# Optimization experiments

Hardware: AMD Instinct MI355X
Metric: run time of the kernel (lower is better)

Reference implementation:

```python
import jax, jax.numpy as jnp
import numpy as np

AH, AW = 7, 7            # alignedHeight, alignedWidth
SCALE = 0.0625           # spatialScale = 1/16


def setup_inputs() -> dict:
    key = jax.random.key(0)
    k1, k2, k3, k4 = jax.random.split(key, 4)
    B, C, H, W, K = 4, 1024, 50, 50, 512
    features = jax.random.normal(k1, (B, C, H, W), dtype=jnp.float32)
    bidx = jax.random.randint(k2, (K, 1), 0, B).astype(jnp.float32)
    xs = jnp.sort(jax.random.uniform(k3, (K, 2), minval=0.0, maxval=799.0), axis=1)
    ys = jnp.sort(jax.random.uniform(k4, (K, 2), minval=0.0, maxval=799.0), axis=1)
    # rois: (batch_idx, x1, y1, x2, y2) in image coords
    rois = jnp.concatenate([bidx, xs[:, 0:1], ys[:, 0:1], xs[:, 1:2], ys[:, 1:2]], axis=1)
    return {"features": features, "rois": rois}


def _roi_align(features, rois):
    # legacy roi_align: grid of (AH+1)x(AW+1) points, bin = extent/(grid-1),
    # one bilinear sample per grid point, zero outside feature map.
    B, C, H, W = features.shape
    bidx = rois[:, 0].astype(jnp.int32)
    x1 = rois[:, 1] * SCALE
    y1 = rois[:, 2] * SCALE
    x2 = rois[:, 3] * SCALE
    y2 = rois[:, 4] * SCALE
    bh = jnp.maximum(y2 - y1, 0.0) / AH  # (AH+1)-1 grid intervals
    bw = jnp.maximum(x2 - x1, 0.0) / AW
    ys = y1[:, None] + jnp.arange(AH + 1, dtype=jnp.float32) * bh[:, None]  # [K,AH+1]
    xs = x1[:, None] + jnp.arange(AW + 1, dtype=jnp.float32) * bw[:, None]  # [K,AW+1]
    yg = ys[:, :, None]   # [K,AH+1,1]
    xg = xs[:, None, :]   # [K,1,AW+1]
    valid = (yg >= 0) & (yg < H) & (xg >= 0) & (xg < W)   # [K,AH+1,AW+1]
    y0 = jnp.clip(jnp.floor(yg), 0, H - 2).astype(jnp.int32)
    x0 = jnp.clip(jnp.floor(xg), 0, W - 2).astype(jnp.int32)
    wy = yg - y0.astype(jnp.float32)  # [K,AH+1,1]
    wx = xg - x0.astype(jnp.float32)  # [K,1,AW+1]
    b = bidx[:, None, None]
    # gathered corners: [K, AH+1, AW+1, C]
    v00 = features[b, :, y0, x0]
    v01 = features[b, :, y0, x0 + 1]
    v10 = features[b, :, y0 + 1, x0]
    v11 = features[b, :, y0 + 1, x0 + 1]
    out = (v00 * ((1 - wy) * (1 - wx))[..., None]
           + v01 * ((1 - wy) * wx)[..., None]
           + v10 * (wy * (1 - wx))[..., None]
           + v11 * (wy * wx)[..., None])
    out = jnp.where(valid[..., None], out, 0.0)
    return jnp.transpose(out, (0, 3, 1, 2))  # [K, C, AH+1, AW+1]


def reference(features, rois):
    a = _roi_align(features, rois)
    # avg_pool2d(kernel=2, stride=1) -> [K, C, AH, AW]
    pooled = (a[..., :-1, :-1] + a[..., 1:, :-1] + a[..., :-1, 1:] + a[..., 1:, 1:]) * 0.25
    return pooled
```

## Files before the change

kernel.cpp:

```cpp
#include <hip/hip_runtime.h>

#define K_ROIS   512
#define BATCH    4
#define CHANNELS 1024
#define FH       50
#define FW       50
#define AH       7
#define AW       7
#define SCALE_F  0.0625f
#define CPT      4


__global__ void roi_prep(const float* __restrict__ rois,
                         int* __restrict__ cnt,
                         int* __restrict__ roiIdx,
                         float4* __restrict__ paramsS) {
    int r = blockIdx.x * blockDim.x + threadIdx.x;
    if (r >= K_ROIS) return;
    float bf = rois[r * 5 + 0];
    float x1 = rois[r * 5 + 1] * SCALE_F;
    float y1 = rois[r * 5 + 2] * SCALE_F;
    float x2 = rois[r * 5 + 3] * SCALE_F;
    float y2 = rois[r * 5 + 4] * SCALE_F;
    float bw = fmaxf(x2 - x1, 0.f) * (1.f / (float)AW);
    float bh = fmaxf(y2 - y1, 0.f) * (1.f / (float)AH);
    int ib = (int)bf;
    int pos = atomicAdd(&cnt[ib], 1);
    roiIdx[ib * K_ROIS + pos] = r;
    paramsS[ib * K_ROIS + pos] = make_float4(x1, y1, bw, bh);
}

__global__ __launch_bounds__(256)
void roi_pool(const float* __restrict__ feat,
              const int* __restrict__ cnt,
              const int* __restrict__ roiIdx,
              const float4* __restrict__ paramsS,
              float* __restrict__ out) {
    __shared__ float4 patch4[FH * FW];

    const int b  = blockIdx.x & 3;
    const int c0 = (blockIdx.x >> 2) * CPT;

    const float* pl = feat + ((size_t)b * CHANNELS + c0) * (FH * FW);
    for (int idx = threadIdx.x; idx < FH * FW; idx += 256) {
        float4 v;
        v.x = pl[idx];
        v.y = pl[idx + FH * FW];
        v.z = pl[idx + 2 * FH * FW];
        v.w = pl[idx + 3 * FH * FW];
        patch4[idx] = v;
    }
    __syncthreads();

    const int lane = threadIdx.x & 63;
    const int wv   = threadIdx.x >> 6;
    const int j = lane >> 3;
    const int i = lane & 7;
    const float jf = (float)j;
    const float iff = (float)i;
    const bool do_out = (j < AH) && (i < AW);
    const int outoff = j * AW + i;

    const int n = cnt[b];
    const int base = b * K_ROIS;

    int rr = wv;
    float4 pp = make_float4(0.f, 0.f, 0.f, 0.f);
    int roi = 0;
    if (rr < n) { pp = paramsS[base + rr]; roi = roiIdx[base + rr]; }

    while (rr < n) {
        const int rn = rr + 4;
        float4 ppn = pp;
        int roin = roi;
        if (rn < n) { ppn = paramsS[base + rn]; roin = roiIdx[base + rn]; }

        const float xg = fmaf(iff, pp.z, pp.x);
        const float yg = fmaf(jf, pp.w, pp.y);
        const bool valid = (yg >= 0.f) && (yg < (float)FH) &&
                           (xg >= 0.f) && (xg < (float)FW);
        const float y0f = fminf(fmaxf(floorf(yg), 0.f), (float)(FH - 2));
        const float x0f = fminf(fmaxf(floorf(xg), 0.f), (float)(FW - 2));
        const float wy = yg - y0f;
        const float wx = xg - x0f;
        const float omwy = 1.f - wy;
        const float omwx = 1.f - wx;
        float w00 = omwy * omwx;
        float w01 = omwy * wx;
        float w10 = wy * omwx;
        float w11 = wy * wx;
        if (!valid) { w00 = 0.f; w01 = 0.f; w10 = 0.f; w11 = 0.f; }
        const int p = (int)y0f * FW + (int)x0f;

        const float4 c00 = patch4[p];
        const float4 c01 = patch4[p + 1];
        const float4 c10 = patch4[p + FW];
        const float4 c11 = patch4[p + FW + 1];

        float4 s;
        s.x = w00 * c00.x + w01 * c01.x + w10 * c10.x + w11 * c11.x;
        s.y = w00 * c00.y + w01 * c01.y + w10 * c10.y + w11 * c11.y;
        s.z = w00 * c00.z + w01 * c01.z + w10 * c10.z + w11 * c11.z;
        s.w = w00 * c00.w + w01 * c01.w + w10 * c10.w + w11 * c11.w;

        float4 t;
        t.x = s.x + __shfl_down(s.x, 1);
        t.y = s.y + __shfl_down(s.y, 1);
        t.z = s.z + __shfl_down(s.z, 1);
        t.w = s.w + __shfl_down(s.w, 1);
        t.x += __shfl_down(t.x, 8);
        t.y += __shfl_down(t.y, 8);
        t.z += __shfl_down(t.z, 8);
        t.w += __shfl_down(t.w, 8);

        if (do_out) {
            const size_t ob = (size_t)roi * (CHANNELS * AH * AW)
                            + (size_t)c0 * (AH * AW) + outoff;
            out[ob]                = t.x * 0.25f;
            out[ob + AH * AW]      = t.y * 0.25f;
            out[ob + 2 * AH * AW]  = t.z * 0.25f;
            out[ob + 3 * AH * AW]  = t.w * 0.25f;
        }

        pp = ppn; roi = roin; rr = rn;
    }
}

extern "C" void kernel_launch(void* const* d_in, const int* in_sizes, int n_in,
                              void* d_out, int out_size, void* d_ws, size_t ws_size,
                              hipStream_t stream) {
    const float* feat = (const float*)d_in[0];
    const float* rois = (const float*)d_in[1];
    float* out = (float*)d_out;

    char* ws = (char*)d_ws;
    int* cnt        = (int*)ws;
    int* roiIdx     = (int*)(ws + 16);
    float4* paramsS = (float4*)(ws + 16 + 4 * K_ROIS * sizeof(int));

    hipMemsetAsync(cnt, 0, 16, stream);
    roi_prep<<<2, 256, 0, stream>>>(rois, cnt, roiIdx, paramsS);
    roi_pool<<<BATCH * (CHANNELS / CPT), 256, 0, stream>>>(feat, cnt, roiIdx, paramsS, out);
}
```

Before: 152.0 us.

## Pack feature patch as fp16 half2 and process eight channels per block

Stores the shared-memory feature patch as packed fp16 (8 channels per 16-byte entry) so each block covers eight channels with 512 threads. Bilinear interpolation and the 2x2 average reduction use packed half2 FMAs, with a DPP lane shift replacing one of the shuffles. This is meant to halve the LDS reads and ALU work per output channel and to amortise the ROI parameter loads over more channels. It gives up accuracy, because intermediate sums are held in fp16, and the per-block patch load becomes larger.

```diff
diff --git a/kernel.cpp b/kernel.cpp
--- a/kernel.cpp
+++ b/kernel.cpp
@@ -1,4 +1,5 @@
 #include <hip/hip_runtime.h>
+#include <hip/hip_fp16.h>
 
 #define K_ROIS   512
 #define BATCH    4
@@ -8,7 +9,7 @@
 #define AH       7
 #define AW       7
 #define SCALE_F  0.0625f
-#define CPT      4
+#define CPT      8
 
 
 __global__ void roi_prep(const float* __restrict__ rois,
@@ -30,25 +31,43 @@
     paramsS[ib * K_ROIS + pos] = make_float4(x1, y1, bw, bh);
 }
 
-__global__ __launch_bounds__(256)
+__device__ __forceinline__ int bci(__half2 h) {
+    union { __half2 h; int i; } u; u.h = h; return u.i;
+}
+__device__ __forceinline__ __half2 bch(unsigned int i) {
+    union { unsigned int i; __half2 h; } u; u.i = i; return u.h;
+}
+__device__ __forceinline__ int dpp_sl1(int x) {
+    return __builtin_amdgcn_update_dpp(0, x, 0x101 , 0xf, 0xf, true);
+}
+
+__global__ __launch_bounds__(512)
 void roi_pool(const float* __restrict__ feat,
               const int* __restrict__ cnt,
               const int* __restrict__ roiIdx,
               const float4* __restrict__ paramsS,
               float* __restrict__ out) {
-    __shared__ float4 patch4[FH * FW];
+    __shared__ uint4 patch4[FH * FW];
 
     const int b  = blockIdx.x & 3;
     const int c0 = (blockIdx.x >> 2) * CPT;
 
     const float* pl = feat + ((size_t)b * CHANNELS + c0) * (FH * FW);
-    for (int idx = threadIdx.x; idx < FH * FW; idx += 256) {
-        float4 v;
-        v.x = pl[idx];
-        v.y = pl[idx + FH * FW];
-        v.z = pl[idx + 2 * FH * FW];
-        v.w = pl[idx + 3 * FH * FW];
-        patch4[idx] = v;
+    for (int idx = threadIdx.x; idx < FH * FW; idx += 512) {
+        float v0 = pl[idx];
+        float v1 = pl[idx + 1 * FH * FW];
+        float v2 = pl[idx + 2 * FH * FW];
+        float v3 = pl[idx + 3 * FH * FW];
+        float v4 = pl[idx + 4 * FH * FW];
+        float v5 = pl[idx + 5 * FH * FW];
+        float v6 = pl[idx + 6 * FH * FW];
+        float v7 = pl[idx + 7 * FH * FW];
+        uint4 pk;
+        pk.x = (unsigned)bci(__floats2half2_rn(v0, v1));
+        pk.y = (unsigned)bci(__floats2half2_rn(v2, v3));
+        pk.z = (unsigned)bci(__floats2half2_rn(v4, v5));
+        pk.w = (unsigned)bci(__floats2half2_rn(v6, v7));
+        patch4[idx] = pk;
     }
     __syncthreads();
 
@@ -70,7 +89,7 @@
     if (rr < n) { pp = paramsS[base + rr]; roi = roiIdx[base + rr]; }
 
     while (rr < n) {
-        const int rn = rr + 4;
+        const int rn = rr + 8;
         float4 ppn = pp;
         int roin = roi;
         if (rn < n) { ppn = paramsS[base + rn]; roin = roiIdx[base + rn]; }
@@ -92,34 +111,50 @@
         if (!valid) { w00 = 0.f; w01 = 0.f; w10 = 0.f; w11 = 0.f; }
         const int p = (int)y0f * FW + (int)x0f;
 
-        const float4 c00 = patch4[p];
-        const float4 c01 = patch4[p + 1];
-        const float4 c10 = patch4[p + FW];
-        const float4 c11 = patch4[p + FW + 1];
+        const uint4 c00 = patch4[p];
+        const uint4 c01 = patch4[p + 1];
+        const uint4 c10 = patch4[p + FW];
+        const uint4 c11 = patch4[p + FW + 1];
 
-        float4 s;
-        s.x = w00 * c00.x + w01 * c01.x + w10 * c10.x + w11 * c11.x;
-        s.y = w00 * c00.y + w01 * c01.y + w10 * c10.y + w11 * c11.y;
-        s.z = w00 * c00.z + w01 * c01.z + w10 * c10.z + w11 * c11.z;
-        s.w = w00 * c00.w + w01 * c01.w + w10 * c10.w + w11 * c11.w;
+        const __half2 W00 = __float2half2_rn(w00);
+        const __half2 W01 = __float2half2_rn(w01);
+        const __half2 W10 = __float2half2_rn(w10);
+        const __half2 W11 = __float2half2_rn(w11);
 
-        float4 t;
-        t.x = s.x + __shfl_down(s.x, 1);
-        t.y = s.y + __shfl_down(s.y, 1);
-        t.z = s.z + __shfl_down(s.z, 1);
-        t.w = s.w + __shfl_down(s.w, 1);
-        t.x += __shfl_down(t.x, 8);
-        t.y += __shfl_down(t.y, 8);
-        t.z += __shfl_down(t.z, 8);
-        t.w += __shfl_down(t.w, 8);
+        __half2 s0 = __hfma2(W00, bch(c00.x), __hfma2(W01, bch(c01.x),
+                     __hfma2(W10, bch(c10.x), __hmul2(W11, bch(c11.x)))));
+        __half2 s1 = __hfma2(W00, bch(c00.y), __hfma2(W01, bch(c01.y),
+                     __hfma2(W10, bch(c10.y), __hmul2(W11, bch(c11.y)))));
+        __half2 s2 = __hfma2(W00, bch(c00.z), __hfma2(W01, bch(c01.z),
+                     __hfma2(W10, bch(c10.z), __hmul2(W11, bch(c11.z)))));
+        __half2 s3 = __hfma2(W00, bch(c00.w), __hfma2(W01, bch(c01.w),
+                     __hfma2(W10, bch(c10.w), __hmul2(W11, bch(c11.w)))));
+
+        __half2 h0 = __hadd2(s0, bch((unsigned)dpp_sl1(bci(s0))));
+        __half2 h1 = __hadd2(s1, bch((unsigned)dpp_sl1(bci(s1))));
+        __half2 h2 = __hadd2(s2, bch((unsigned)dpp_sl1(bci(s2))));
+        __half2 h3 = __hadd2(s3, bch((unsigned)dpp_sl1(bci(s3))));
+
+        __half2 t0 = __hadd2(h0, bch((unsigned)__shfl_down(bci(h0), 8)));
+        __half2 t1 = __hadd2(h1, bch((unsigned)__shfl_down(bci(h1), 8)));
+        __half2 t2 = __hadd2(h2, bch((unsigned)__shfl_down(bci(h2), 8)));
+        __half2 t3 = __hadd2(h3, bch((unsigned)__shfl_down(bci(h3), 8)));
 
         if (do_out) {
             const size_t ob = (size_t)roi * (CHANNELS * AH * AW)
                             + (size_t)c0 * (AH * AW) + outoff;
-            out[ob]                = t.x * 0.25f;
-            out[ob + AH * AW]      = t.y * 0.25f;
-            out[ob + 2 * AH * AW]  = t.z * 0.25f;
-            out[ob + 3 * AH * AW]  = t.w * 0.25f;
+            float2 f0 = __half22float2(t0);
+            float2 f1 = __half22float2(t1);
+            float2 f2 = __half22float2(t2);
+            float2 f3 = __half22float2(t3);
+            out[ob + 0 * AH * AW] = f0.x * 0.25f;
+            out[ob + 1 * AH * AW] = f0.y * 0.25f;
+            out[ob + 2 * AH * AW] = f1.x * 0.25f;
+            out[ob + 3 * AH * AW] = f1.y * 0.25f;
+            out[ob + 4 * AH * AW] = f2.x * 0.25f;
+            out[ob + 5 * AH * AW] = f2.y * 0.25f;
+            out[ob + 6 * AH * AW] = f3.x * 0.25f;
+            out[ob + 7 * AH * AW] = f3.y * 0.25f;
         }
 
         pp = ppn; roi = roin; rr = rn;
@@ -140,5 +175,5 @@
 
     hipMemsetAsync(cnt, 0, 16, stream);
     roi_prep<<<2, 256, 0, stream>>>(rois, cnt, roiIdx, paramsS);
-    roi_pool<<<BATCH * (CHANNELS / CPT), 256, 0, stream>>>(feat, cnt, roiIdx, paramsS, out);
+    roi_pool<<<BATCH * (CHANNELS / CPT), 512, 0, stream>>>(feat, cnt, roiIdx, paramsS, out);
 }
```

After: 144.1 us. 1.05x faster.
